# Kernel optimization log

Hardware: AMD Instinct MI355X
Metric: run time of the kernel (lower is better)

The kernel has to match this reference:

```python
import jax, jax.numpy as jnp
import numpy as np

D = 768  # inputdim = k_size = v_size (forced equal by residual + LayerNorm)
B, T = 16, 2048


def setup_inputs() -> dict:
    key = jax.random.key(0)
    ks = jax.random.split(key, 9)
    s = 1.0 / np.sqrt(D)
    return {
        "x": jax.random.normal(ks[0], (B, T, D), dtype=jnp.float32),
        "Wk": jax.random.normal(ks[1], (D, D), dtype=jnp.float32) * s,
        "bk": jnp.zeros((D,), dtype=jnp.float32),
        "Wq": jax.random.normal(ks[2], (D, D), dtype=jnp.float32) * s,
        "bq": jnp.zeros((D,), dtype=jnp.float32),
        "Wv": jax.random.normal(ks[3], (D, D), dtype=jnp.float32) * s,
        "bv": jnp.zeros((D,), dtype=jnp.float32),
        "gamma": jnp.ones((D,), dtype=jnp.float32),
        "beta": jnp.zeros((D,), dtype=jnp.float32),
    }


def reference(x, Wk, bk, Wq, bq, Wv, bv, gamma, beta):
    sq_k = jnp.sqrt(jnp.asarray(D, dtype=x.dtype))
    keys = jnp.einsum("btd,kd->btk", x, Wk) + bk      # [B,T,K]
    queries = jnp.einsum("btd,kd->btk", x, Wq) + bq   # [B,T,K]
    values = jnp.einsum("btd,vd->btv", x, Wv) + bv    # [B,T,V]
    logits = jnp.einsum("bqk,btk->bqt", queries, keys)  # [B,Tq,Tk]
    # NB: original softmaxes over dim=1 (the QUERY axis), then scales AFTER softmax
    q_k = jax.nn.softmax(logits, axis=1) / sq_k
    applied = jnp.einsum("bqt,btv->bqv", q_k, values)  # [B,T,V]
    y = applied + x
    mu = jnp.mean(y, axis=-1, keepdims=True)
    var = jnp.mean(jnp.square(y - mu), axis=-1, keepdims=True)
    return (y - mu) * jax.lax.rsqrt(var + 1e-5) * gamma + beta
```

## Files before the change

kernel.cpp:

```cpp
#include <hip/hip_runtime.h>
#include <hip/hip_fp16.h>

#define DD 768
#define BB 16
#define TT 2048
#define BT (BB*TT)
#define NQS 8
#define BST 76

using f16 = _Float16;
typedef __attribute__((ext_vector_type(8))) f16 half8;
typedef __attribute__((ext_vector_type(4))) f16 half4;
typedef __attribute__((ext_vector_type(4))) float f32x4;

#define GSWZ(r) ((((r) & 3)) ^ (((r) >> 2) & 3))

typedef const __attribute__((address_space(1))) unsigned int* gas1;
typedef __attribute__((address_space(3))) unsigned int* las3;
__device__ __forceinline__ void gload16(const void* g, void* l){
  __builtin_amdgcn_global_load_lds((gas1)g, (las3)l, 16, 0, 0);
}

__global__ __launch_bounds__(256)
void tofp16_kernel(const float* __restrict__ src, f16* __restrict__ dst, int n4){
  const int stride = gridDim.x * 256;
  for (int i = blockIdx.x*256 + threadIdx.x; i < n4; i += stride){
    float4 v = ((const float4*)src)[i];
    half4 h; h[0]=(f16)v.x; h[1]=(f16)v.y; h[2]=(f16)v.z; h[3]=(f16)v.w;
    ((half4*)dst)[i] = h;
  }
}

__global__ __launch_bounds__(256)
void wconv_kernel(const float* __restrict__ w0, const float* __restrict__ w1,
                  const float* __restrict__ w2, f16* __restrict__ dst){
  const float* src = blockIdx.y == 0 ? w0 : blockIdx.y == 1 ? w1 : w2;
  f16* d = dst + (size_t)blockIdx.y * DD * DD;
  const int n4 = DD*DD/4;
  const int stride = gridDim.x * 256;
  for (int i = blockIdx.x*256 + threadIdx.x; i < n4; i += stride){
    float4 v = ((const float4*)src)[i];
    half4 h; h[0]=(f16)v.x; h[1]=(f16)v.y; h[2]=(f16)v.z; h[3]=(f16)v.w;
    ((half4*)d)[i] = h;
  }
}

template<int OMODE>
__global__ __launch_bounds__(256, OMODE==2 ? 3 : 2)
void gemmk(const f16* __restrict__ A, int lda, long sA,
           const f16* __restrict__ B, int ldb, long sB,
           void* __restrict__ Out, int ldc, long sC,
           const float* __restrict__ aux, int Kdim,
           float* __restrict__ f0, float* __restrict__ f1,
           const f16* __restrict__ cs, f16* __restrict__ vt)
{
  constexpr int MR = (OMODE==2) ? 4 : 8;
  constexpr int BM = MR * 32;
  constexpr int AC = BM / 64;

  __shared__ f16 lA[3][BM*32];
  __shared__ f16 lB[3][128*32];
  __shared__ float smx[OMODE==1 ? 4 : 1][4][16], szx[OMODE==1 ? 4 : 1][4][16];
  __shared__ f16 lCC[OMODE==2 ? 2048 : 8];

  const int nx = gridDim.x, ny = gridDim.y, nwg = nx * ny, cpx = nwg >> 3;
  int h = blockIdx.x + nx * blockIdx.y;
  h = (h & 7) * cpx + (h >> 3);
  const int bx = h / ny, by = h % ny;

  const int b = blockIdx.z;
  const f16* A_ = A + (size_t)b * sA;
  const f16* B_ = B + (size_t)b * sB;
  const int m0 = bx * BM, n0 = by * 128;
  const int tid = threadIdx.x, lane = tid & 63, wave = tid >> 6;
  const int wm = wave >> 1, wn = wave & 1;

  size_t gaO[AC], gbO[2];
#pragma unroll
  for (int k = 0; k < AC; ++k){
    int c = k*256 + tid, r = c >> 2, s = (c & 3) ^ GSWZ(r);
    gaO[k] = (size_t)(m0 + r) * lda + s * 8;
  }
#pragma unroll
  for (int k = 0; k < 2; ++k){
    int c = k*256 + tid, r = c >> 2, s = (c & 3) ^ GSWZ(r);
    gbO[k] = (size_t)(n0 + r) * ldb + s * 8;
  }

  f32x4 acc[MR][4] = {};
  const int NT = Kdim >> 5;

  auto STAGE = [&](int u, int kt){
#pragma unroll
    for (int k = 0; k < AC; ++k) gload16(A_ + gaO[k] + kt, &lA[u][(k*256+tid)*8]);
#pragma unroll
    for (int k = 0; k < 2; ++k)  gload16(B_ + gbO[k] + kt, &lB[u][(k*256+tid)*8]);
  };

  if constexpr (OMODE == 2){
    const f16* cb = cs + ((size_t)b * NQS + (bx >> 1)) * TT;
    ((half8*)lCC)[tid] = ((const half8*)cb)[tid];
    __syncthreads();
  }

  STAGE(0, 0); STAGE(1, 32);

  const int frow = lane & 15;
  const int rsl = (((lane >> 4) ^ GSWZ(frow)) & 3) * 8;
  const int tsl = (lane >> 4) * 8;
  const int offA = (wm*(MR*16) + frow)*32 + rsl;
  const int offB = (wn*64 + frow)*32 + rsl;

  int u = 0;
  for (int t = 0; t < NT; ++t){
    int u2 = u + 2; if (u2 >= 3) u2 -= 3;
    __builtin_amdgcn_s_barrier();
    __builtin_amdgcn_sched_barrier(0);
    if (t + 2 < NT) STAGE(u2, (t + 2) * 32);
    const int rem = NT - 1 - t;
    if constexpr (AC == 4){
      if (rem >= 2)      asm volatile("s_waitcnt vmcnt(12)" ::: "memory");
      else if (rem == 1) asm volatile("s_waitcnt vmcnt(6)"  ::: "memory");
      else               asm volatile("s_waitcnt vmcnt(0)"  ::: "memory");
    } else {
      if (rem >= 2)      asm volatile("s_waitcnt vmcnt(8)" ::: "memory");
      else if (rem == 1) asm volatile("s_waitcnt vmcnt(4)" ::: "memory");
      else               asm volatile("s_waitcnt vmcnt(0)" ::: "memory");
    }
    __builtin_amdgcn_s_barrier();
    __builtin_amdgcn_sched_barrier(0);

    const f16* tA = &lA[u][0] + offA;
    const f16* tB = &lB[u][0] + offB;
    half8 af[MR], bf[4];
#pragma unroll
    for (int i = 0; i < MR; ++i) af[i] = *(const half8*)(tA + i*512);
#pragma unroll
    for (int j = 0; j < 4; ++j)  bf[j] = *(const half8*)(tB + j*512);
    if constexpr (OMODE == 2){
      half8 cc = *(const half8*)&lCC[t*32 + tsl];
#pragma unroll
      for (int i = 0; i < MR; ++i) af[i] *= cc;
    }
    __builtin_amdgcn_s_setprio(1);
#pragma unroll
    for (int i = 0; i < MR; ++i)
#pragma unroll
      for (int j = 0; j < 4; ++j)
        acc[i][j] = __builtin_amdgcn_mfma_f32_16x16x32_f16(af[i], bf[j], acc[i][j], 0,0,0);
    __builtin_amdgcn_s_setprio(0);
    u = (u + 1 == 3) ? 0 : u + 1;
  }

  __syncthreads();
  const int kq4 = (lane >> 4) * 4;
  f16* bnc = &lA[0][0] + wave * (16*BST);
  const int rrow = lane >> 2, rcol = (lane & 3) * 16;

  if constexpr (OMODE == 0 || OMODE == 2){
    const int plane = (OMODE == 0) ? (by / 6) : 0;
    const int nloc0 = (OMODE == 0) ? (n0 - plane * DD) : n0;
    const bool toVt = (OMODE == 0) && (plane == 2);
    float bias4[4] = {};
    if constexpr (OMODE == 0){
#pragma unroll
      for (int j = 0; j < 4; ++j) bias4[j] = aux[n0 + wn*64 + j*16 + frow];
    }
    f16* O = (f16*)Out + (OMODE == 0 ? (size_t)plane * sC : (size_t)b * sC);
#pragma unroll
    for (int i = 0; i < MR; ++i){
#pragma unroll
      for (int j = 0; j < 4; ++j)
#pragma unroll
        for (int r = 0; r < 4; ++r)
          bnc[(kq4 + r)*BST + j*16 + frow] = (f16)(acc[i][j][r] + bias4[j]);
      if (!toVt){
        half8 w0 = *(const half8*)&bnc[rrow*BST + rcol];
        half8 w1 = *(const half8*)&bnc[rrow*BST + rcol + 8];
        const int gr = m0 + wm*(MR*16) + i*16 + rrow;
        const int gc = nloc0 + wn*64 + rcol;
        *(half8*)&O[(size_t)gr*ldc + gc]     = w0;
        *(half8*)&O[(size_t)gr*ldc + gc + 8] = w1;
      } else {
        f16 tmp[16];
#pragma unroll
        for (int k = 0; k < 16; ++k) tmp[k] = bnc[k*BST + lane];
        half8 v0, v1;
#pragma unroll
        for (int k = 0; k < 8; ++k){ v0[k] = tmp[k]; v1[k] = tmp[8+k]; }
        const int tokg = m0 + wm*(MR*16) + i*16;
        const int batch = tokg >> 11, tok = tokg & (TT-1);
        f16* Vo = vt + ((size_t)batch*DD + nloc0 + wn*64 + lane)*TT + tok;
        *(half8*)&Vo[0] = v0;
        *(half8*)&Vo[8] = v1;
      }
    }
  } else {
    f16* O = (f16*)Out + (size_t)b * sC;
    float Mb[4];
#pragma unroll
    for (int j = 0; j < 4; ++j){
      float mx = acc[0][j][0];
#pragma unroll
      for (int i = 0; i < MR; ++i)
#pragma unroll
        for (int r = 0; r < 4; ++r) mx = fmaxf(mx, acc[i][j][r]);
      mx = fmaxf(mx, __shfl_xor(mx, 16, 64));
      mx = fmaxf(mx, __shfl_xor(mx, 32, 64));
      if (lane < 16) smx[wave][j][lane] = mx;
      Mb[j] = mx;
    }
    __syncthreads();
#pragma unroll
    for (int j = 0; j < 4; ++j)
      Mb[j] = fmaxf(Mb[j], smx[wave ^ 2][j][frow]);
    float zz[4] = {};
#pragma unroll
    for (int i = 0; i < MR; ++i){
#pragma unroll
      for (int j = 0; j < 4; ++j)
#pragma unroll
        for (int r = 0; r < 4; ++r){
          float e = __expf(acc[i][j][r] - Mb[j]);
          zz[j] += e;
          bnc[(kq4 + r)*BST + j*16 + frow] = (f16)e;
        }
      half8 w0 = *(const half8*)&bnc[rrow*BST + rcol];
      half8 w1 = *(const half8*)&bnc[rrow*BST + rcol + 8];
      const int gr = m0 + wm*(MR*16) + i*16 + rrow;
      const int gc = n0 + wn*64 + rcol;
      *(half8*)&O[(size_t)gr*ldc + gc]     = w0;
      *(half8*)&O[(size_t)gr*ldc + gc + 8] = w1;
    }
#pragma unroll
    for (int j = 0; j < 4; ++j){
      zz[j] += __shfl_xor(zz[j], 16, 64);
      zz[j] += __shfl_xor(zz[j], 32, 64);
      if (lane < 16) szx[wave][j][lane] = zz[j];
    }
    __syncthreads();
    if (wm == 0 && lane < 16){
#pragma unroll
      for (int j = 0; j < 4; ++j){
        const int gc = n0 + wn*64 + j*16 + lane;
        size_t o = ((size_t)b * NQS + bx) * TT + gc;
        f0[o] = Mb[j];
        f1[o] = zz[j] + szx[wave + 2][j][lane];
      }
    }
  }
}

__global__ __launch_bounds__(256)
void statsB_kernel(const float* __restrict__ pm, const float* __restrict__ pz,
                   f16* __restrict__ c){
  const int b = blockIdx.y;
  const int t = blockIdx.x * 256 + threadIdx.x;
  float am[NQS], az[NQS];
#pragma unroll
  for (int k = 0; k < NQS; ++k){
    size_t o = ((size_t)b * NQS + k) * TT + t;
    am[k] = pm[o]; az[k] = pz[o];
  }
  float M = am[0];
#pragma unroll
  for (int k = 1; k < NQS; ++k) M = fmaxf(M, am[k]);
  float Z = 0.f;
#pragma unroll
  for (int k = 0; k < NQS; ++k) Z += az[k] * __expf(am[k] - M);
  const float zi = 1.f / (Z * 27.712812921102035f);
#pragma unroll
  for (int k = 0; k < NQS; ++k)
    c[((size_t)b * NQS + k) * TT + t] = (f16)(__expf(am[k] - M) * zi);
}

__global__ __launch_bounds__(192)
void ln2_kernel(const half4* __restrict__ applied, const half4* __restrict__ xf,
                const float4* __restrict__ gamma4, const float4* __restrict__ beta4,
                float4* __restrict__ out){
  const size_t base = (size_t)blockIdx.x * (DD/4);
  const int cc = threadIdx.x;
  half4 a4 = applied[base + cc];
  half4 x4 = xf[base + cc];
  float y0 = (float)a4[0] + (float)x4[0];
  float y1 = (float)a4[1] + (float)x4[1];
  float y2 = (float)a4[2] + (float)x4[2];
  float y3 = (float)a4[3] + (float)x4[3];
  float s = y0+y1+y2+y3;
  float sq = y0*y0+y1*y1+y2*y2+y3*y3;
#pragma unroll
  for (int off = 32; off > 0; off >>= 1){
    s  += __shfl_down(s,  off, 64);
    sq += __shfl_down(sq, off, 64);
  }
  __shared__ float rs_[3], rq_[3];
  const int lane = threadIdx.x & 63, w = threadIdx.x >> 6;
  if (lane == 0){ rs_[w] = s; rq_[w] = sq; }
  __syncthreads();
  const float S_ = rs_[0]+rs_[1]+rs_[2];
  const float Q_ = rq_[0]+rq_[1]+rq_[2];
  const float mu  = S_ * (1.f/DD);
  const float var = Q_ * (1.f/DD) - mu*mu;
  const float rstd = rsqrtf(var + 1e-5f);
  float4 g = gamma4[cc], be = beta4[cc], o;
  o.x = (y0 - mu)*rstd*g.x + be.x;
  o.y = (y1 - mu)*rstd*g.y + be.y;
  o.z = (y2 - mu)*rstd*g.z + be.z;
  o.w = (y3 - mu)*rstd*g.w + be.w;
  out[base + cc] = o;
}

extern "C" void kernel_launch(void* const* d_in, const int* in_sizes, int n_in,
                              void* d_out, int out_size, void* d_ws, size_t ws_size,
                              hipStream_t stream)
{
  const float* x    = (const float*)d_in[0];
  const float* Wk   = (const float*)d_in[1];
  const float* bk   = (const float*)d_in[2];
  const float* Wq   = (const float*)d_in[3];
  const float* bq   = (const float*)d_in[4];
  const float* Wv   = (const float*)d_in[5];
  const float* bv   = (const float*)d_in[6];
  const float* gamma= (const float*)d_in[7];
  const float* beta = (const float*)d_in[8];
  float* out = (float*)d_out;

  const size_t PW = (size_t)DD*DD*2;
  const size_t PB = (size_t)TT*DD*2;
  const size_t T4 = (size_t)TT*4;
  auto al = [](size_t n){ return (n + 255) & ~(size_t)255; };

  auto need = [&](int G)->size_t{
    size_t t = al(3*PW) + al(3*DD*4) + al((size_t)BB*PB) + al((size_t)BB*TT*TT*2)
             + al((size_t)BB*PB) + al(2*(size_t)G*PB)
             + 2*al((size_t)G*NQS*T4) + al((size_t)BB*NQS*TT*2);
    if (2*(size_t)G*PB < (size_t)BB*PB) t += al((size_t)BB*PB);
    return t;
  };

  int G = 0;
  for (int g : {16, 8, 4, 2, 1}) if (need(g) <= ws_size){ G = g; break; }
  if (G == 0) return;

  char* p = (char*)d_ws;
  auto alloc = [&](size_t n)->char*{ char* r = p; p += (n + 255) & ~(size_t)255; return r; };
  f16*   Wf    = (f16*)alloc(3*PW);
  float* biasf = (float*)alloc(3*DD*4);
  f16*   Vt    = (f16*)alloc((size_t)BB*PB);
  f16*   P16   = (f16*)alloc((size_t)BB*TT*TT*2);
  f16*   Xf    = (f16*)alloc((size_t)BB*PB);
  f16*   QKVc  = (f16*)alloc(2*(size_t)G*PB);
  float* pm    = (float*)alloc((size_t)G*NQS*T4);
  float* pz    = (float*)alloc((size_t)G*NQS*T4);
  f16*   cbuf  = (f16*)alloc((size_t)BB*NQS*TT*2);
  f16* applied = (2*(size_t)G*PB >= (size_t)BB*PB) ? QKVc
               : (f16*)alloc((size_t)BB*PB);
  f16* Qc = QKVc, *Kc = QKVc + (size_t)G*TT*DD;

  wconv_kernel<<<dim3(288, 3), 256, 0, stream>>>(Wq, Wk, Wv, Wf);
  hipMemcpyAsync(biasf,        bq, DD*4, hipMemcpyDeviceToDevice, stream);
  hipMemcpyAsync(biasf +   DD, bk, DD*4, hipMemcpyDeviceToDevice, stream);
  hipMemcpyAsync(biasf + 2*DD, bv, DD*4, hipMemcpyDeviceToDevice, stream);
  tofp16_kernel<<<2048, 256, 0, stream>>>(x, Xf, BT*DD/4);

  const int nRows = G * TT;
  for (int b0 = 0; b0 < BB; b0 += G){
    dim3 gp(nRows/256, 3*DD/128, 1);
    gemmk<0><<<gp, 256, 0, stream>>>(Xf + (size_t)b0*TT*DD, DD, 0,
                                     Wf, DD, 0,
                                     QKVc, DD, (long)G*TT*DD, biasf, DD,
                                     nullptr, nullptr, nullptr,
                                     Vt + (size_t)b0*DD*TT);

    dim3 gs(TT/256, TT/128, G);
    gemmk<1><<<gs, 256, 0, stream>>>(Qc, DD, (long)TT*DD, Kc, DD, (long)TT*DD,
                                     P16 + (size_t)b0*TT*TT, TT, (long)TT*TT,
                                     nullptr, DD, pm, pz, nullptr, nullptr);

    statsB_kernel<<<dim3(TT/256, G), 256, 0, stream>>>(
        pm, pz, cbuf + (size_t)b0*NQS*TT);
  }

  dim3 gpv(TT/128, DD/128, BB);
  gemmk<2><<<gpv, 256, 0, stream>>>(P16, TT, (long)TT*TT, Vt, TT, (long)DD*TT,
                                    applied, DD, (long)TT*DD, nullptr, TT,
                                    nullptr, nullptr, cbuf, nullptr);

  ln2_kernel<<<BT, 192, 0, stream>>>((const half4*)applied, (const half4*)Xf,
                                     (const float4*)gamma, (const float4*)beta,
                                     (float4*)out);
}
```

Measured before the change: 515.8 us.

## Switch GEMM inner loop from 16x16x32 to 32x32x16 MFMA tiles

Replaces the 16x16x32 f16 MFMA fragments with 32x32x16 MFMA in the shared GEMM kernel, which changes the LDS fragment loading, the accumulator layout, and the epilogue index mapping for the bias store, the V-transpose store and the softmax max/sum reductions. Larger MFMA tiles need fewer LDS fragment reads per FLOP and fewer cross-lane shuffles in the reductions. The cost is a more intricate epilogue register-to-row mapping and possible register pressure from the 16-wide accumulators.

```diff
diff --git a/kernel.cpp b/kernel.cpp
--- a/kernel.cpp
+++ b/kernel.cpp
@@ -9,9 +9,9 @@
 #define BST 76
 
 using f16 = _Float16;
-typedef __attribute__((ext_vector_type(8))) f16 half8;
-typedef __attribute__((ext_vector_type(4))) f16 half4;
-typedef __attribute__((ext_vector_type(4))) float f32x4;
+typedef __attribute__((ext_vector_type(8)))  f16 half8;
+typedef __attribute__((ext_vector_type(4)))  f16 half4;
+typedef __attribute__((ext_vector_type(16))) float f32x16;
 
 #define GSWZ(r) ((((r) & 3)) ^ (((r) >> 2) & 3))
 
@@ -54,13 +54,13 @@
            float* __restrict__ f0, float* __restrict__ f1,
            const f16* __restrict__ cs, f16* __restrict__ vt)
 {
-  constexpr int MR = (OMODE==2) ? 4 : 8;
-  constexpr int BM = MR * 32;
+  constexpr int FI = (OMODE==2) ? 2 : 4;
+  constexpr int BM = FI * 64;
   constexpr int AC = BM / 64;
 
   __shared__ f16 lA[3][BM*32];
   __shared__ f16 lB[3][128*32];
-  __shared__ float smx[OMODE==1 ? 4 : 1][4][16], szx[OMODE==1 ? 4 : 1][4][16];
+  __shared__ float smx[OMODE==1 ? 4 : 1][2][32], szx[OMODE==1 ? 4 : 1][2][32];
   __shared__ f16 lCC[OMODE==2 ? 2048 : 8];
 
   const int nx = gridDim.x, ny = gridDim.y, nwg = nx * ny, cpx = nwg >> 3;
@@ -87,7 +87,7 @@
     gbO[k] = (size_t)(n0 + r) * ldb + s * 8;
   }
 
-  f32x4 acc[MR][4] = {};
+  f32x16 acc2[FI][2] = {};
   const int NT = Kdim >> 5;
 
   auto STAGE = [&](int u, int kt){
@@ -105,11 +105,12 @@
 
   STAGE(0, 0); STAGE(1, 32);
 
-  const int frow = lane & 15;
-  const int rsl = (((lane >> 4) ^ GSWZ(frow)) & 3) * 8;
-  const int tsl = (lane >> 4) * 8;
-  const int offA = (wm*(MR*16) + frow)*32 + rsl;
-  const int offB = (wn*64 + frow)*32 + rsl;
+  const int row31 = lane & 31, khalf = lane >> 5;
+  const int g = GSWZ(row31);
+  const int slA = (wm*(FI*32) + row31)*32;
+  const int slB = (wn*64 + row31)*32;
+  const int s0 = ((khalf)     ^ g) * 8;
+  const int s1 = ((2 + khalf) ^ g) * 8;
 
   int u = 0;
   for (int t = 0; t < NT; ++t){
@@ -130,122 +131,141 @@
     __builtin_amdgcn_s_barrier();
     __builtin_amdgcn_sched_barrier(0);
 
-    const f16* tA = &lA[u][0] + offA;
-    const f16* tB = &lB[u][0] + offB;
-    half8 af[MR], bf[4];
-#pragma unroll
-    for (int i = 0; i < MR; ++i) af[i] = *(const half8*)(tA + i*512);
-#pragma unroll
-    for (int j = 0; j < 4; ++j)  bf[j] = *(const half8*)(tB + j*512);
+    const f16* LA = &lA[u][0];
+    const f16* LB = &lB[u][0];
+    half8 aF[FI][2], bF[2][2];
+#pragma unroll
+    for (int fi = 0; fi < FI; ++fi){
+      aF[fi][0] = *(const half8*)(LA + slA + fi*1024 + s0);
+      aF[fi][1] = *(const half8*)(LA + slA + fi*1024 + s1);
+    }
+#pragma unroll
+    for (int fj = 0; fj < 2; ++fj){
+      bF[fj][0] = *(const half8*)(LB + slB + fj*1024 + s0);
+      bF[fj][1] = *(const half8*)(LB + slB + fj*1024 + s1);
+    }
     if constexpr (OMODE == 2){
-      half8 cc = *(const half8*)&lCC[t*32 + tsl];
-#pragma unroll
-      for (int i = 0; i < MR; ++i) af[i] *= cc;
+      half8 cc0 = *(const half8*)&lCC[t*32 + khalf*8];
+      half8 cc1 = *(const half8*)&lCC[t*32 + 16 + khalf*8];
+#pragma unroll
+      for (int fi = 0; fi < FI; ++fi){ aF[fi][0] *= cc0; aF[fi][1] *= cc1; }
     }
     __builtin_amdgcn_s_setprio(1);
 #pragma unroll
-    for (int i = 0; i < MR; ++i)
-#pragma unroll
-      for (int j = 0; j < 4; ++j)
-        acc[i][j] = __builtin_amdgcn_mfma_f32_16x16x32_f16(af[i], bf[j], acc[i][j], 0,0,0);
+    for (int fi = 0; fi < FI; ++fi)
+#pragma unroll
+      for (int fj = 0; fj < 2; ++fj){
+        acc2[fi][fj] = __builtin_amdgcn_mfma_f32_32x32x16_f16(aF[fi][0], bF[fj][0], acc2[fi][fj], 0,0,0);
+        acc2[fi][fj] = __builtin_amdgcn_mfma_f32_32x32x16_f16(aF[fi][1], bF[fj][1], acc2[fi][fj], 0,0,0);
+      }
     __builtin_amdgcn_s_setprio(0);
     u = (u + 1 == 3) ? 0 : u + 1;
   }
 
   __syncthreads();
-  const int kq4 = (lane >> 4) * 4;
   f16* bnc = &lA[0][0] + wave * (16*BST);
-  const int rrow = lane >> 2, rcol = (lane & 3) * 16;
+  const int rr = lane >> 2, sB4 = lane & 3;
 
   if constexpr (OMODE == 0 || OMODE == 2){
     const int plane = (OMODE == 0) ? (by / 6) : 0;
     const int nloc0 = (OMODE == 0) ? (n0 - plane * DD) : n0;
     const bool toVt = (OMODE == 0) && (plane == 2);
-    float bias4[4] = {};
+    float bias2[2] = {};
     if constexpr (OMODE == 0){
 #pragma unroll
-      for (int j = 0; j < 4; ++j) bias4[j] = aux[n0 + wn*64 + j*16 + frow];
+      for (int fj = 0; fj < 2; ++fj) bias2[fj] = aux[n0 + wn*64 + fj*32 + row31];
     }
     f16* O = (f16*)Out + (OMODE == 0 ? (size_t)plane * sC : (size_t)b * sC);
 #pragma unroll
-    for (int i = 0; i < MR; ++i){
-#pragma unroll
-      for (int j = 0; j < 4; ++j)
-#pragma unroll
-        for (int r = 0; r < 4; ++r)
-          bnc[(kq4 + r)*BST + j*16 + frow] = (f16)(acc[i][j][r] + bias4[j]);
-      if (!toVt){
-        half8 w0 = *(const half8*)&bnc[rrow*BST + rcol];
-        half8 w1 = *(const half8*)&bnc[rrow*BST + rcol + 8];
-        const int gr = m0 + wm*(MR*16) + i*16 + rrow;
-        const int gc = nloc0 + wn*64 + rcol;
-        *(half8*)&O[(size_t)gr*ldc + gc]     = w0;
-        *(half8*)&O[(size_t)gr*ldc + gc + 8] = w1;
-      } else {
-        f16 tmp[16];
-#pragma unroll
-        for (int k = 0; k < 16; ++k) tmp[k] = bnc[k*BST + lane];
-        half8 v0, v1;
-#pragma unroll
-        for (int k = 0; k < 8; ++k){ v0[k] = tmp[k]; v1[k] = tmp[8+k]; }
-        const int tokg = m0 + wm*(MR*16) + i*16;
-        const int batch = tokg >> 11, tok = tokg & (TT-1);
-        f16* Vo = vt + ((size_t)batch*DD + nloc0 + wn*64 + lane)*TT + tok;
-        *(half8*)&Vo[0] = v0;
-        *(half8*)&Vo[8] = v1;
+    for (int fi = 0; fi < FI; ++fi)
+#pragma unroll
+      for (int oct = 0; oct < 2; ++oct){
+#pragma unroll
+        for (int fj = 0; fj < 2; ++fj)
+#pragma unroll
+          for (int r8 = 0; r8 < 8; ++r8){
+            const int reg = oct*8 + r8;
+            const int rl = (r8&3) + 8*(r8>>2) + 4*khalf;
+            bnc[rl*BST + fj*32 + row31] = (f16)(acc2[fi][fj][reg] + bias2[fj]);
+          }
+        if (!toVt){
+#pragma unroll
+          for (int it = 0; it < 2; ++it){
+            const int sIdx = sB4 + 4*it;
+            half8 w = *(const half8*)&bnc[rr*BST + sIdx*8];
+            const int gr = m0 + wm*(FI*32) + fi*32 + oct*16 + rr;
+            const int gc = nloc0 + wn*64 + sIdx*8;
+            *(half8*)&O[(size_t)gr*ldc + gc] = w;
+          }
+        } else {
+          f16 tmp[16];
+#pragma unroll
+          for (int k = 0; k < 16; ++k) tmp[k] = bnc[k*BST + lane];
+          half8 v0, v1;
+#pragma unroll
+          for (int k = 0; k < 8; ++k){ v0[k] = tmp[k]; v1[k] = tmp[8+k]; }
+          const int tokg = m0 + wm*(FI*32) + fi*32 + oct*16;
+          const int batch = tokg >> 11, tok = tokg & (TT-1);
+          f16* Vo = vt + ((size_t)batch*DD + nloc0 + wn*64 + lane)*TT + tok;
+          *(half8*)&Vo[0] = v0;
+          *(half8*)&Vo[8] = v1;
+        }
       }
-    }
   } else {
     f16* O = (f16*)Out + (size_t)b * sC;
-    float Mb[4];
-#pragma unroll
-    for (int j = 0; j < 4; ++j){
-      float mx = acc[0][j][0];
-#pragma unroll
-      for (int i = 0; i < MR; ++i)
-#pragma unroll
-        for (int r = 0; r < 4; ++r) mx = fmaxf(mx, acc[i][j][r]);
-      mx = fmaxf(mx, __shfl_xor(mx, 16, 64));
+    float Mb2[2];
+#pragma unroll
+    for (int fj = 0; fj < 2; ++fj){
+      float mx = acc2[0][fj][0];
+#pragma unroll
+      for (int fi = 0; fi < FI; ++fi)
+#pragma unroll
+        for (int reg = 0; reg < 16; ++reg) mx = fmaxf(mx, acc2[fi][fj][reg]);
       mx = fmaxf(mx, __shfl_xor(mx, 32, 64));
-      if (lane < 16) smx[wave][j][lane] = mx;
-      Mb[j] = mx;
+      if (lane < 32) smx[wave][fj][lane] = mx;
+      Mb2[fj] = mx;
     }
     __syncthreads();
 #pragma unroll
-    for (int j = 0; j < 4; ++j)
-      Mb[j] = fmaxf(Mb[j], smx[wave ^ 2][j][frow]);
-    float zz[4] = {};
-#pragma unroll
-    for (int i = 0; i < MR; ++i){
-#pragma unroll
-      for (int j = 0; j < 4; ++j)
-#pragma unroll
-        for (int r = 0; r < 4; ++r){
-          float e = __expf(acc[i][j][r] - Mb[j]);
-          zz[j] += e;
-          bnc[(kq4 + r)*BST + j*16 + frow] = (f16)e;
+    for (int fj = 0; fj < 2; ++fj)
+      Mb2[fj] = fmaxf(Mb2[fj], smx[wave ^ 2][fj][row31]);
+    float zz2[2] = {0.f, 0.f};
+#pragma unroll
+    for (int fi = 0; fi < FI; ++fi)
+#pragma unroll
+      for (int oct = 0; oct < 2; ++oct){
+#pragma unroll
+        for (int fj = 0; fj < 2; ++fj)
+#pragma unroll
+          for (int r8 = 0; r8 < 8; ++r8){
+            const int reg = oct*8 + r8;
+            const int rl = (r8&3) + 8*(r8>>2) + 4*khalf;
+            float e = __expf(acc2[fi][fj][reg] - Mb2[fj]);
+            zz2[fj] += e;
+            bnc[rl*BST + fj*32 + row31] = (f16)e;
+          }
+#pragma unroll
+        for (int it = 0; it < 2; ++it){
+          const int sIdx = sB4 + 4*it;
+          half8 w = *(const half8*)&bnc[rr*BST + sIdx*8];
+          const int gr = m0 + wm*(FI*32) + fi*32 + oct*16 + rr;
+          const int gc = n0 + wn*64 + sIdx*8;
+          *(half8*)&O[(size_t)gr*ldc + gc] = w;
         }
-      half8 w0 = *(const half8*)&bnc[rrow*BST + rcol];
-      half8 w1 = *(const half8*)&bnc[rrow*BST + rcol + 8];
-      const int gr = m0 + wm*(MR*16) + i*16 + rrow;
-      const int gc = n0 + wn*64 + rcol;
-      *(half8*)&O[(size_t)gr*ldc + gc]     = w0;
-      *(half8*)&O[(size_t)gr*ldc + gc + 8] = w1;
-    }
-#pragma unroll
-    for (int j = 0; j < 4; ++j){
-      zz[j] += __shfl_xor(zz[j], 16, 64);
-      zz[j] += __shfl_xor(zz[j], 32, 64);
-      if (lane < 16) szx[wave][j][lane] = zz[j];
+      }
+#pragma unroll
+    for (int fj = 0; fj < 2; ++fj){
+      zz2[fj] += __shfl_xor(zz2[fj], 32, 64);
+      if (lane < 32) szx[wave][fj][lane] = zz2[fj];
     }
     __syncthreads();
-    if (wm == 0 && lane < 16){
-#pragma unroll
-      for (int j = 0; j < 4; ++j){
-        const int gc = n0 + wn*64 + j*16 + lane;
+    if (wm == 0 && lane < 32){
+#pragma unroll
+      for (int fj = 0; fj < 2; ++fj){
+        const int gc = n0 + wn*64 + fj*32 + lane;
         size_t o = ((size_t)b * NQS + bx) * TT + gc;
-        f0[o] = Mb[j];
-        f1[o] = zz[j] + szx[wave + 2][j][lane];
+        f0[o] = Mb2[fj];
+        f1[o] = zz2[fj] + szx[wave + 2][fj][lane];
       }
     }
   }
```

After: 534.2 us. 3.6% more time.
